# Performance work log

Measured on AMD Instinct MI355X. Metric: run time of the kernel, lower is better.

The kernel has to match this reference:

```python
import jax, jax.numpy as jnp
import numpy as np

B, C, H, W = 32, 512, 28, 28
NUM_CLASSES = 200
THRESHOLD = 0.6


def _conv(x, w, b, pad):
    y = jax.lax.conv_general_dilated(
        x, w, window_strides=(1, 1), padding=[(pad, pad), (pad, pad)],
        dimension_numbers=('NCHW', 'OIHW', 'NCHW'))
    return y + b[None, :, None, None]


def _classifier(x, w1, b1, w2, b2, w3, b3):
    x = jax.nn.relu(_conv(x, w1, b1, 1))
    x = jax.nn.relu(_conv(x, w2, b2, 1))
    return _conv(x, w3, b3, 0)


def _avg_pool3(x):
    # torch F.avg_pool2d(k=3, stride=1, pad=1, count_include_pad=True): sum window / 9
    s = jax.lax.reduce_window(x, 0.0, jax.lax.add, (1, 1, 3, 3), (1, 1, 1, 1),
                              [(0, 0), (0, 0), (1, 1), (1, 1)])
    return s / 9.0


def setup_inputs() -> dict:
    key = jax.random.key(0)
    ks = jax.random.split(key, 16)
    sc = 0.02
    inp = {
        'x': jax.random.normal(ks[0], (B, C, H, W), jnp.float32),
        'label': jax.random.randint(ks[1], (B, NUM_CLASSES), 0, 2),
        'w1a': jax.random.normal(ks[2], (1024, 512, 3, 3), jnp.float32) * sc,
        'b1a': jax.random.normal(ks[3], (1024,), jnp.float32) * sc,
        'w2a': jax.random.normal(ks[4], (1024, 1024, 3, 3), jnp.float32) * sc,
        'b2a': jax.random.normal(ks[5], (1024,), jnp.float32) * sc,
        'w3a': jax.random.normal(ks[6], (NUM_CLASSES, 1024, 1, 1), jnp.float32) * sc,
        'b3a': jax.random.normal(ks[7], (NUM_CLASSES,), jnp.float32) * sc,
        'w1b': jax.random.normal(ks[8], (1024, 512, 3, 3), jnp.float32) * sc,
        'b1b': jax.random.normal(ks[9], (1024,), jnp.float32) * sc,
        'w2b': jax.random.normal(ks[10], (1024, 1024, 3, 3), jnp.float32) * sc,
        'b2b': jax.random.normal(ks[11], (1024,), jnp.float32) * sc,
        'w3b': jax.random.normal(ks[12], (NUM_CLASSES, 1024, 1, 1), jnp.float32) * sc,
        'b3b': jax.random.normal(ks[13], (NUM_CLASSES,), jnp.float32) * sc,
    }
    return inp


def reference(x, label, w1a, b1a, w2a, b2a, w3a, b3a,
              w1b, b1b, w2b, b2b, w3b, b3b):
    feats = _avg_pool3(x)                       # [B,512,H,W]
    out_A = _classifier(feats, w1a, b1a, w2a, b2a, w3a, b3a)  # [B,K,H,W]
    logits_A = out_A.mean(axis=(2, 3))          # [B,K]

    # attention map: per-sample max over channels whose label is nonzero,
    # floored at 0 (the loop seeds the channel stack with a zeros map)
    sel = jnp.where(label[:, :, None, None] > 0, out_A, -jnp.inf)
    atten = jnp.maximum(sel.max(axis=1), 0.0)   # [B,H,W]

    # per-sample min-max normalization over HxW
    mins = atten.min(axis=(1, 2), keepdims=True)
    maxs = atten.max(axis=(1, 2), keepdims=True)
    atten_n = (atten - mins) / (maxs - mins)

    # threshold-erase mask (constant w.r.t. autograd, matching torch code)
    mask = jax.lax.stop_gradient(jnp.where(atten_n >= THRESHOLD, 0.0, 1.0))
    feats_erased = feats * mask[:, None, :, :]

    out_B = _classifier(feats_erased, w1b, b1b, w2b, b2b, w3b, b3b)
    logits_B = out_B.mean(axis=(2, 3))
    return logits_A, logits_B
```

## Files before the change

### kernel.cpp

```cpp
#include <hip/hip_runtime.h>
#include <hip/hip_bf16.h>

typedef unsigned long long ull;
typedef __attribute__((ext_vector_type(8))) short short8;
typedef __attribute__((ext_vector_type(8))) __bf16 bf16x8;
typedef __attribute__((ext_vector_type(4))) float floatx4;

#define GLL16(gp, lp) __builtin_amdgcn_global_load_lds( \
  (__attribute__((address_space(1))) void*)(gp), \
  (__attribute__((address_space(3))) void*)(lp), 16, 0, 0)

#define WVM(N) asm volatile("s_waitcnt vmcnt(" #N ")" ::: "memory")

__device__ __forceinline__ floatx4 mfma16(short8 a, short8 b, floatx4 c){
  return __builtin_amdgcn_mfma_f32_16x16x32_bf16(
      __builtin_bit_cast(bf16x8, a), __builtin_bit_cast(bf16x8, b), c, 0, 0, 0);
}

__device__ __forceinline__ unsigned pkbf(float a, float b){
  unsigned ua = __float_as_uint(a), ub = __float_as_uint(b);
  ua += 0x7fffu + ((ua >> 16) & 1u);
  ub += 0x7fffu + ((ub >> 16) & 1u);
  return (ua >> 16) | (ub & 0xffff0000u);
}

__global__ __launch_bounds__(256) void pool_kernel(const float* __restrict__ x,
                                                   unsigned short* __restrict__ out){
  __shared__ float xs[16*784];
  const int tid = threadIdx.x;
  const int b = blockIdx.x >> 5, cg = blockIdx.x & 31;
  const float* src = x + ((size_t)b*512 + cg*16)*784;
  for (int i=tid;i<16*784;i+=256) xs[i]=src[i];
  __syncthreads();
  unsigned* dst = (unsigned*)out + ((size_t)b*960)*256 + cg*8;
  for (int o=tid;o<30*32*8;o+=256){
    int cip = o & 7, pos = o >> 3;
    int row = pos >> 5, col = pos & 31;
    float s0=0.f, s1=0.f;
    if (row>=1 && row<=28 && col>=1 && col<=28){
      int h=row-1, w=col-1;
      const float* p0 = &xs[(cip*2)*784];
      const float* p1 = p0 + 784;
      #pragma unroll
      for (int dh=-1;dh<=1;++dh){ int hh=h+dh; if ((unsigned)hh<28u){
        #pragma unroll
        for (int dw=-1;dw<=1;++dw){ int ww=w+dw; if((unsigned)ww<28u){
          s0 += p0[hh*28+ww]; s1 += p1[hh*28+ww]; } } } }
      s0 /= 9.f; s1 /= 9.f;
    }
    dst[(size_t)pos*256 + cip] = pkbf(s0, s1);
  }
}

template<int CIN>
__global__ __launch_bounds__(256) void prep3x3(const float* __restrict__ w,
                                               unsigned short* __restrict__ Wt){
  __shared__ float wsm[CIN*9];
  const int co = blockIdx.x, tid = threadIdx.x;
  const float* src = w + (size_t)co*(CIN*9);
  for (int i=tid;i<CIN*9;i+=256) wsm[i]=src[i];
  __syncthreads();
  for (int o=tid;o<9*(CIN/2);o+=256){
    int t = o/(CIN/2), cp = o - t*(CIN/2);
    unsigned v = pkbf(wsm[(cp*2)*9+t], wsm[(cp*2+1)*9+t]);
    ((unsigned*)Wt)[(((size_t)t*1024+co)*CIN>>1) + cp] = v;
  }
}

__global__ __launch_bounds__(256) void prep1x1(const float* __restrict__ w3,
                                               unsigned short* __restrict__ Wp){
  const int row = blockIdx.x, tid = threadIdx.x;
  unsigned* dst = (unsigned*)Wp + (size_t)row*512;
  if (row < 200){
    const float* src = w3 + (size_t)row*1024;
    for (int j=tid;j<512;j+=256) dst[j] = pkbf(src[2*j], src[2*j+1]);
  } else {
    for (int j=tid;j<512;j+=256) dst[j] = 0u;
  }
}

template<int CIN>
__global__ __launch_bounds__(256, 2) void conv3x3_v8(
    const unsigned short* __restrict__ X,
    const unsigned short* __restrict__ Wt,
    const float* __restrict__ bias,
    unsigned short* __restrict__ Out)
{
  constexpr int NCH = CIN/32;
  constexpr size_t CB = (size_t)CIN*2;
  constexpr size_t TAPSTR = (size_t)1024*CB;
  __shared__ char Als[32768];
  __shared__ char Bls[40960];

  const int tid = threadIdx.x;
  const int l = tid & 63, wv = tid >> 6;
  const int cog = wv & 1, pg = wv >> 1;
  const int bid = blockIdx.x;
  const int co0 = (bid & 7) << 7;
  const int y = bid >> 3;
  const int b = y >> 2, rb = y & 3;
  const int r0 = rb << 3;
  const bool active = (pg == 0) || (rb < 3);

  const int sbyt = (l*16) ^ (((l>>3)&7)<<4);
  const int srow = sbyt >> 6;
  const int sw   = sbyt & 63;

  const ull aS0 = (ull)Wt + (size_t)(co0 + (wv*2)*16   + srow)*CB + sw;
  const ull aS1 = (ull)Wt + (size_t)(co0 + (wv*2+1)*16 + srow)*CB + sw;
  ull bS[5];
  #pragma unroll
  for (int k=0;k<5;++k){
    int q = (wv + 4*k)*16 + srow;
    int trow = q >> 5, tcol = q & 31;
    int ir = r0 + trow; if (ir > 29) ir = 29;
    bS[k] = (ull)X + ((size_t)b*960 + ir*32 + tcol)*CB + sw;
  }

  const int jl = l & 15, g = l >> 4;
  int paE[4];
  #pragma unroll
  for (int m=0;m<4;++m){
    int xo = (cog*64 + m*16 + jl)*64 + g*16;
    paE[m] = xo ^ (((xo>>7)&7)<<4);
  }
  int pbS[3][7];
  #pragma unroll
  for (int f=0;f<7;++f){
    int p = pg*112 + f*16 + jl;
    int hl = p/28, cl = p - hl*28;
    #pragma unroll
    for (int ss=0;ss<3;++ss){
      int xo = (hl*32 + cl + ss)*64 + g*16;
      pbS[ss][f] = xo ^ (((xo>>7)&7)<<4);
    }
  }

  floatx4 acc[4][7];
  #pragma unroll
  for (int m=0;m<4;++m)
    #pragma unroll
    for (int f=0;f<7;++f) acc[m][f] = (floatx4){0.f,0.f,0.f,0.f};

  #pragma unroll
  for (int k=0;k<5;++k) GLL16((const void*)bS[k], Bls + (wv + 4*k)*1024);
  #pragma unroll
  for (int pp=0;pp<3;++pp){
    const int tap = pp, slot = pp;
    GLL16((const void*)(aS0 + (size_t)tap*TAPSTR), Als + slot*8192 + (wv*2)*1024);
    GLL16((const void*)(aS1 + (size_t)tap*TAPSTR), Als + slot*8192 + (wv*2+1)*1024);
  }

  #pragma unroll 1
  for (int c=0;c<NCH;++c){
    const char* Bp = Bls + (c&1)*20480;
    #pragma unroll
    for (int t=0;t<9;++t){
      const int rr = t/3, ss = t - rr*3;
      if (t == 0){
        #pragma unroll
        for (int k=0;k<5;++k)
          GLL16((const void*)(bS[k] + (size_t)(c+1)*64),
                Bls + ((c+1)&1)*20480 + (wv + 4*k)*1024);
      }
      {
        const int stTap = (t<6) ? t+3 : t-6;
        const size_t aoff = (size_t)stTap*TAPSTR + (size_t)(c + (t>=6))*64;
        const int sd = ((c + t + 3) & 3)*8192;
        GLL16((const void*)(aS0 + aoff), Als + sd + (wv*2)*1024);
        GLL16((const void*)(aS1 + aoff), Als + sd + (wv*2+1)*1024);
      }
      if (t <= 2) { WVM(11); } else { WVM(6); }
      __builtin_amdgcn_s_barrier();
      if (active){
        const char* ap = Als + ((c + t) & 3)*8192;
        short8 a0 = *(const short8*)(ap + paE[0]);
        short8 a1 = *(const short8*)(ap + paE[1]);
        short8 a2 = *(const short8*)(ap + paE[2]);
        short8 a3 = *(const short8*)(ap + paE[3]);
        short8 bv[7];
        #pragma unroll
        for (int f=0;f<7;++f)
          bv[f] = *(const short8*)(Bp + (pbS[ss][f] + rr*2048));
        __builtin_amdgcn_s_setprio(1);
        #pragma unroll
        for (int f=0;f<7;++f){
          acc[0][f] = mfma16(a0, bv[f], acc[0][f]);
          acc[1][f] = mfma16(a1, bv[f], acc[1][f]);
          acc[2][f] = mfma16(a2, bv[f], acc[2][f]);
          acc[3][f] = mfma16(a3, bv[f], acc[3][f]);
        }
        __builtin_amdgcn_s_setprio(0);
      }
      __builtin_amdgcn_s_barrier();
    }
  }

  if (!active) return;

  #pragma unroll
  for (int m=0;m<4;++m){
    const int coL = cog*64 + m*16 + g*4;
    const float4 bv4 = *(const float4*)&bias[co0 + coL];
    #pragma unroll
    for (int f=0;f<7;++f){
      int pp = pg*112 + f*16 + jl;
      int hl = pp/28, cl = pp - hl*28;
      float v0 = fmaxf(acc[m][f][0] + bv4.x, 0.f);
      float v1 = fmaxf(acc[m][f][1] + bv4.y, 0.f);
      float v2 = fmaxf(acc[m][f][2] + bv4.z, 0.f);
      float v3 = fmaxf(acc[m][f][3] + bv4.w, 0.f);
      uint2 pk; pk.x = pkbf(v0,v1); pk.y = pkbf(v2,v3);
      size_t oa = ((size_t)b*960 + (size_t)(r0 + hl + 1)*32 + (cl + 1))*1024 + (co0 + coL);
      *(uint2*)(Out + oa) = pk;
    }
  }
}

template<int CIN, bool K3, bool BF16OUT>
__global__ __launch_bounds__(512, 2) void conv_mfma(
    const unsigned short* __restrict__ X,
    const unsigned short* __restrict__ Wt,
    const float* __restrict__ bias, int biasN,
    void* __restrict__ Out)
{
  constexpr int T9 = K3 ? 9 : 1;
  constexpr int NA = K3 ? 9 : 1;
  __shared__ short Als[T9*4096];
  __shared__ short Bls[10240];
  __shared__ float biasLs[128];

  const int tid = threadIdx.x;
  const int l = tid & 63, wv = tid >> 6;
  const int wc = wv & 3, wp = wv >> 2;
  const int co0 = blockIdx.x << 7;
  const int by = blockIdx.y;
  const int b = by >> 2, rb = by & 3;
  const int r0 = rb << 3;
  const int nrh = (rb < 3) ? 10 : 6;
  const int NB = 2*nrh;
  const bool active = (wp == 0) || (rb < 3);

  if (tid < 128) biasLs[tid] = (co0 + tid < biasN) ? bias[co0 + tid] : 0.f;

  const size_t laneOff = (size_t)(l >> 2)*(CIN*2) + (size_t)(l & 3)*16;

  ull aB[NA];
  #pragma unroll
  for (int j=0;j<NA;++j){
    int k = wv*NA + j;
    int t = K3 ? (k >> 3) : 0;
    int cog2 = K3 ? (k & 7) : k;
    aB[j] = (ull)Wt + ((size_t)(t*1024 + co0 + cog2*16)*(CIN*2)) + laneOff;
  }
  const ull xBase = (ull)X + ((size_t)b*960)*(CIN*2) + (size_t)(r0*32)*(CIN*2) + laneOff;
  ull bB0=0, bB1=0, bB2=0; int nb=0;
  if (wv < NB)      { bB0 = xBase + (size_t)(wv*16)*(CIN*2);      nb = 1; }
  if (wv + 8 < NB)  { bB1 = xBase + (size_t)((wv+8)*16)*(CIN*2);  nb = 2; }
  if (wv + 16 < NB) { bB2 = xBase + (size_t)((wv+16)*16)*(CIN*2); nb = 3; }

  const int jl = l & 15, g = l >> 4;
  int paE[2];
  #pragma unroll
  for (int m=0;m<2;++m) paE[m] = (wc*32 + m*16 + jl)*32 + g*8;
  int pbE[7], ph[7], pc[7];
  #pragma unroll
  for (int f=0;f<7;++f){
    int p = wp*112 + f*16 + jl;
    int hl = p / 28, cl = p - hl*28;
    ph[f]=hl; pc[f]=cl;
    pbE[f] = (hl*32 + cl)*32 + g*8;
  }

  floatx4 acc[2][7];
  #pragma unroll
  for (int m=0;m<2;++m)
    #pragma unroll
    for (int f=0;f<7;++f) acc[m][f] = (floatx4){0.f,0.f,0.f,0.f};

  const int NCH = CIN/32;
  for (int c=0;c<NCH;++c){
    if (c) __syncthreads();
    const size_t cOff = (size_t)c*64;
    #pragma unroll
    for (int j=0;j<NA;++j)
      GLL16((const void*)(aB[j] + cOff), (char*)Als + (wv*NA + j)*1024);
    GLL16((const void*)(bB0 + cOff), (char*)Bls + wv*1024);
    if (nb > 1) GLL16((const void*)(bB1 + cOff), (char*)Bls + (wv+8)*1024);
    if (nb > 2) GLL16((const void*)(bB2 + cOff), (char*)Bls + (wv+16)*1024);
    __syncthreads();
    if (active){
      #pragma unroll
      for (int t=0;t<T9;++t){
        const int tA = t*4096;
        const int tB = K3 ? (((t/3)*32 + (t - (t/3)*3))*32) : ((1*32+1)*32);
        short8 a0 = *(const short8*)&Als[tA + paE[0]];
        short8 a1 = *(const short8*)&Als[tA + paE[1]];
        #pragma unroll
        for (int f=0;f<7;++f){
          short8 bvv = *(const short8*)&Bls[tB + pbE[f]];
          acc[0][f] = mfma16(a0, bvv, acc[0][f]);
          acc[1][f] = mfma16(a1, bvv, acc[1][f]);
        }
      }
    }
  }

  if (!active) return;

  #pragma unroll
  for (int m=0;m<2;++m){
    const int coL = wc*32 + m*16 + g*4;
    const float4 bv4 = *(const float4*)&biasLs[coL];
    #pragma unroll
    for (int f=0;f<7;++f){
      float v0 = acc[m][f][0] + bv4.x;
      float v1 = acc[m][f][1] + bv4.y;
      float v2 = acc[m][f][2] + bv4.z;
      float v3 = acc[m][f][3] + bv4.w;
      if constexpr (BF16OUT){
        v0=fmaxf(v0,0.f); v1=fmaxf(v1,0.f); v2=fmaxf(v2,0.f); v3=fmaxf(v3,0.f);
        uint2 pk; pk.x = pkbf(v0,v1); pk.y = pkbf(v2,v3);
        size_t oa = ((size_t)b*960 + (size_t)(r0 + ph[f] + 1)*32 + (pc[f]+1))*1024 + (co0 + coL);
        *(uint2*)((unsigned short*)Out + oa) = pk;
      } else {
        int co = co0 + coL;
        if (co < 200){
          int p = wp*112 + f*16 + jl;
          size_t oa = ((size_t)b*784 + (size_t)(r0*28) + p)*200 + co;
          float4 ov; ov.x=v0; ov.y=v1; ov.z=v2; ov.w=v3;
          *(float4*)((float*)Out + oa) = ov;
        }
      }
    }
  }
}

__global__ __launch_bounds__(256) void logits_kernel(const float* __restrict__ outC,
                                                     float* __restrict__ dst){
  const int b = blockIdx.x, seg = blockIdx.y;
  const int co = threadIdx.x;
  if (co >= 200) return;
  const float* base = outC + ((size_t)b*784 + seg*98)*200 + co;
  float s = 0.f;
  for (int p=0;p<98;++p) s += base[(size_t)p*200];
  atomicAdd(&dst[b*200+co], s*(1.f/784.f));
}

__global__ __launch_bounds__(256) void atten_kernel(const float* __restrict__ outC,
                                                    const int* __restrict__ label,
                                                    float* __restrict__ mask){
  __shared__ float al[784];
  __shared__ float redn[256], redx[256];
  __shared__ unsigned char lab[200];
  const int b = blockIdx.x, tid = threadIdx.x;
  for (int i=tid;i<200;i+=256) lab[i] = label[b*200+i] > 0 ? 1 : 0;
  __syncthreads();
  for (int p=tid;p<784;p+=256){
    const float* row = outC + ((size_t)b*784+p)*200;
    float m = -__builtin_inff();
    for (int c=0;c<200;++c) if (lab[c]) m = fmaxf(m, row[c]);
    al[p] = fmaxf(m, 0.f);
  }
  __syncthreads();
  float mn = __builtin_inff(), mx = -__builtin_inff();
  for (int p=tid;p<784;p+=256){ float v=al[p]; mn=fminf(mn,v); mx=fmaxf(mx,v); }
  redn[tid]=mn; redx[tid]=mx; __syncthreads();
  for (int s2=128;s2>0;s2>>=1){
    if (tid<s2){ redn[tid]=fminf(redn[tid],redn[tid+s2]); redx[tid]=fmaxf(redx[tid],redx[tid+s2]); }
    __syncthreads();
  }
  mn = redn[0]; mx = redx[0];
  for (int p=tid;p<784;p+=256){
    float nrm = (al[p]-mn)/(mx-mn);
    mask[b*784+p] = (nrm >= 0.6f) ? 0.f : 1.f;
  }
}

__global__ __launch_bounds__(256) void erase_kernel(const unsigned short* __restrict__ feats,
                                                    const float* __restrict__ mask,
                                                    unsigned short* __restrict__ dst){
  const int blk = blockIdx.x; const int b = blk/30, row = blk - b*30;
  const size_t base = ((size_t)b*960 + row*32)*512;
  for (int i=threadIdx.x; i<4096; i+=256){
    int col = i >> 7;
    float mv = 0.f;
    if (row>=1 && row<=28 && col>=1 && col<=28) mv = mask[b*784 + (row-1)*28 + (col-1)];
    uint2 v = make_uint2(0u,0u);
    if (mv > 0.5f) v = *(const uint2*)(feats + base + (size_t)i*4);
    *(uint2*)(dst + base + (size_t)i*4) = v;
  }
}

extern "C" void kernel_launch(void* const* d_in, const int* in_sizes, int n_in,
                              void* d_out, int out_size, void* d_ws, size_t ws_size,
                              hipStream_t stream){
  (void)in_sizes; (void)n_in; (void)out_size; (void)ws_size;
  const float* x   = (const float*)d_in[0];
  const int* label = (const int*)d_in[1];
  const float* w1a = (const float*)d_in[2];  const float* b1a = (const float*)d_in[3];
  const float* w2a = (const float*)d_in[4];  const float* b2a = (const float*)d_in[5];
  const float* w3a = (const float*)d_in[6];  const float* b3a = (const float*)d_in[7];
  const float* w1b = (const float*)d_in[8];  const float* b1b = (const float*)d_in[9];
  const float* w2b = (const float*)d_in[10]; const float* b2b = (const float*)d_in[11];
  const float* w3b = (const float*)d_in[12]; const float* b3b = (const float*)d_in[13];

  char* ws = (char*)d_ws;
  unsigned short* WtS = (unsigned short*)(ws);
  unsigned short* WtL = (unsigned short*)(ws + 9441280);
  unsigned short* W3p = (unsigned short*)(ws + 28319744);
  unsigned short* F   = (unsigned short*)(ws + 28848128);
  unsigned short* G1  = (unsigned short*)(ws + 60309504);
  unsigned short* G2  = (unsigned short*)(ws + 123228160);
  float* outC  = (float*)(ws + 186146816);
  float* maskB = (float*)(ws + 206217216);
  float* logA = (float*)d_out;
  float* logB = logA + 6400;

  hipMemsetAsync(G1, 0, 62914560, stream);
  hipMemsetAsync(G2, 0, 62914560, stream);
  hipMemsetAsync(d_out, 0, 51200, stream);

  pool_kernel<<<1024,256,0,stream>>>(x, F);

  prep3x3<512><<<1024,256,0,stream>>>(w1a, WtS);
  conv3x3_v8<512><<<1024,256,0,stream>>>(F, WtS, b1a, G1);
  prep3x3<1024><<<1024,256,0,stream>>>(w2a, WtL);
  conv3x3_v8<1024><<<1024,256,0,stream>>>(G1, WtL, b2a, G2);
  prep1x1<<<256,256,0,stream>>>(w3a, W3p);
  conv_mfma<1024,false,false><<<dim3(2,128),512,0,stream>>>(G2, W3p, b3a, 200, outC);
  logits_kernel<<<dim3(32,8),256,0,stream>>>(outC, logA);
  atten_kernel<<<32,256,0,stream>>>(outC, label, maskB);
  erase_kernel<<<960,256,0,stream>>>(F, maskB, G1);

  prep3x3<512><<<1024,256,0,stream>>>(w1b, WtS);
  conv3x3_v8<512><<<1024,256,0,stream>>>(G1, WtS, b1b, G2);
  prep3x3<1024><<<1024,256,0,stream>>>(w2b, WtL);
  conv3x3_v8<1024><<<1024,256,0,stream>>>(G2, WtL, b2b, G1);
  prep1x1<<<256,256,0,stream>>>(w3b, W3p);
  conv_mfma<1024,false,false><<<dim3(2,128),512,0,stream>>>(G1, W3p, b3b, 200, outC);
  logits_kernel<<<dim3(32,8),256,0,stream>>>(outC, logB);
}
```

Measured before the change: 1.510 ms.

## Double K-chunk to 64 channels and restructure conv3x3 pipeline to double buffers

The 3x3 conv kernel now processes 64 input channels per chunk instead of 32. That halves the number of outer chunk iterations and doubles the MFMA work done per barrier. The weight-tile ring of four 8KB slots becomes two 16KB ping-pong buffers, each prefetched one tap ahead. The input tile is single-buffered at 40KB and reloaded after all nine taps of a chunk, with a wait and barrier at the start of the next chunk. Every tap now waits for all outstanding loads (vmcnt 0), which removes the deeper prefetch distance and may expose memory latency, especially when the input tile is refilled.

New measurement: 1.460 ms. 1.03x faster.

```diff
diff --git a/kernel.cpp b/kernel.cpp
--- a/kernel.cpp
+++ b/kernel.cpp
@@ -80,13 +80,13 @@
 }
 
 template<int CIN>
-__global__ __launch_bounds__(256, 2) void conv3x3_v8(
+__global__ __launch_bounds__(256, 2) void conv3x3_v9(
     const unsigned short* __restrict__ X,
     const unsigned short* __restrict__ Wt,
     const float* __restrict__ bias,
     unsigned short* __restrict__ Out)
 {
-  constexpr int NCH = CIN/32;
+  constexpr int NCH = CIN/64;
   constexpr size_t CB = (size_t)CIN*2;
   constexpr size_t TAPSTR = (size_t)1024*CB;
   __shared__ char Als[32768];
@@ -102,16 +102,18 @@
   const int r0 = rb << 3;
   const bool active = (pg == 0) || (rb < 3);
 
-  const int sbyt = (l*16) ^ (((l>>3)&7)<<4);
-  const int srow = sbyt >> 6;
-  const int sw   = sbyt & 63;
-
-  const ull aS0 = (ull)Wt + (size_t)(co0 + (wv*2)*16   + srow)*CB + sw;
-  const ull aS1 = (ull)Wt + (size_t)(co0 + (wv*2+1)*16 + srow)*CB + sw;
-  ull bS[5];
-  #pragma unroll
-  for (int k=0;k<5;++k){
-    int q = (wv + 4*k)*16 + srow;
+  const int sb = (l*16) ^ (((l>>3)&7)<<4);
+  const int sr = sb >> 7;
+  const int sw = sb & 127;
+
+  ull aS[4];
+  #pragma unroll
+  for (int k=0;k<4;++k)
+    aS[k] = (ull)Wt + (size_t)(co0 + (wv*4+k)*8 + sr)*CB + sw;
+  ull bS[10];
+  #pragma unroll
+  for (int k=0;k<10;++k){
+    int q = (wv + 4*k)*8 + sr;
     int trow = q >> 5, tcol = q & 31;
     int ir = r0 + trow; if (ir > 29) ir = 29;
     bS[k] = (ull)X + ((size_t)b*960 + ir*32 + tcol)*CB + sw;
@@ -121,7 +123,7 @@
   int paE[4];
   #pragma unroll
   for (int m=0;m<4;++m){
-    int xo = (cog*64 + m*16 + jl)*64 + g*16;
+    int xo = (cog*64 + m*16 + jl)*128 + g*16;
     paE[m] = xo ^ (((xo>>7)&7)<<4);
   }
   int pbS[3][7];
@@ -131,7 +133,7 @@
     int hl = p/28, cl = p - hl*28;
     #pragma unroll
     for (int ss=0;ss<3;++ss){
-      int xo = (hl*32 + cl + ss)*64 + g*16;
+      int xo = (hl*32 + cl + ss)*128 + g*16;
       pbS[ss][f] = xo ^ (((xo>>7)&7)<<4);
     }
   }
@@ -143,56 +145,59 @@
     for (int f=0;f<7;++f) acc[m][f] = (floatx4){0.f,0.f,0.f,0.f};
 
   #pragma unroll
-  for (int k=0;k<5;++k) GLL16((const void*)bS[k], Bls + (wv + 4*k)*1024);
-  #pragma unroll
-  for (int pp=0;pp<3;++pp){
-    const int tap = pp, slot = pp;
-    GLL16((const void*)(aS0 + (size_t)tap*TAPSTR), Als + slot*8192 + (wv*2)*1024);
-    GLL16((const void*)(aS1 + (size_t)tap*TAPSTR), Als + slot*8192 + (wv*2+1)*1024);
-  }
+  for (int k=0;k<10;++k) GLL16((const void*)bS[k], Bls + (wv + 4*k)*1024);
+  #pragma unroll
+  for (int k=0;k<4;++k)  GLL16((const void*)aS[k], Als + (wv*4+k)*1024);
+  WVM(0);
+  __builtin_amdgcn_s_barrier();
 
   #pragma unroll 1
   for (int c=0;c<NCH;++c){
-    const char* Bp = Bls + (c&1)*20480;
     #pragma unroll
     for (int t=0;t<9;++t){
       const int rr = t/3, ss = t - rr*3;
-      if (t == 0){
+      const int cur = ((c + t) & 1)*16384;
+      const int nxt = cur ^ 16384;
+      const int ntap = (t<8) ? t+1 : 0;
+      const size_t aoff = (size_t)ntap*TAPSTR + (size_t)(t<8 ? c : c+1)*128;
+      #pragma unroll
+      for (int k=0;k<4;++k)
+        GLL16((const void*)(aS[k] + aoff), Als + nxt + (wv*4+k)*1024);
+      if (t == 0 && c > 0){
+        WVM(4);
+        __builtin_amdgcn_s_barrier();
+      }
+      if (active){
         #pragma unroll
-        for (int k=0;k<5;++k)
-          GLL16((const void*)(bS[k] + (size_t)(c+1)*64),
-                Bls + ((c+1)&1)*20480 + (wv + 4*k)*1024);
+        for (int ks=0;ks<2;++ks){
+          const int kx = ks*64;
+          const char* ap = Als + cur;
+          short8 a0 = *(const short8*)(ap + (paE[0]^kx));
+          short8 a1 = *(const short8*)(ap + (paE[1]^kx));
+          short8 a2 = *(const short8*)(ap + (paE[2]^kx));
+          short8 a3 = *(const short8*)(ap + (paE[3]^kx));
+          short8 bv[7];
+          #pragma unroll
+          for (int f=0;f<7;++f)
+            bv[f] = *(const short8*)(Bls + ((pbS[ss][f]^kx) + rr*4096));
+          __builtin_amdgcn_s_setprio(1);
+          #pragma unroll
+          for (int f=0;f<7;++f){
+            acc[0][f] = mfma16(a0, bv[f], acc[0][f]);
+            acc[1][f] = mfma16(a1, bv[f], acc[1][f]);
+            acc[2][f] = mfma16(a2, bv[f], acc[2][f]);
+            acc[3][f] = mfma16(a3, bv[f], acc[3][f]);
+          }
+          __builtin_amdgcn_s_setprio(0);
+        }
       }
-      {
-        const int stTap = (t<6) ? t+3 : t-6;
-        const size_t aoff = (size_t)stTap*TAPSTR + (size_t)(c + (t>=6))*64;
-        const int sd = ((c + t + 3) & 3)*8192;
-        GLL16((const void*)(aS0 + aoff), Als + sd + (wv*2)*1024);
-        GLL16((const void*)(aS1 + aoff), Als + sd + (wv*2+1)*1024);
-      }
-      if (t <= 2) { WVM(11); } else { WVM(6); }
+      WVM(0);
       __builtin_amdgcn_s_barrier();
-      if (active){
-        const char* ap = Als + ((c + t) & 3)*8192;
-        short8 a0 = *(const short8*)(ap + paE[0]);
-        short8 a1 = *(const short8*)(ap + paE[1]);
-        short8 a2 = *(const short8*)(ap + paE[2]);
-        short8 a3 = *(const short8*)(ap + paE[3]);
-        short8 bv[7];
-        #pragma unroll
-        for (int f=0;f<7;++f)
-          bv[f] = *(const short8*)(Bp + (pbS[ss][f] + rr*2048));
-        __builtin_amdgcn_s_setprio(1);
-        #pragma unroll
-        for (int f=0;f<7;++f){
-          acc[0][f] = mfma16(a0, bv[f], acc[0][f]);
-          acc[1][f] = mfma16(a1, bv[f], acc[1][f]);
-          acc[2][f] = mfma16(a2, bv[f], acc[2][f]);
-          acc[3][f] = mfma16(a3, bv[f], acc[3][f]);
-        }
-        __builtin_amdgcn_s_setprio(0);
-      }
-      __builtin_amdgcn_s_barrier();
+    }
+    if (c + 1 < NCH){
+      #pragma unroll
+      for (int k=0;k<10;++k)
+        GLL16((const void*)(bS[k] + (size_t)(c+1)*128), Bls + (wv + 4*k)*1024);
     }
   }
 
@@ -424,9 +429,9 @@
   pool_kernel<<<1024,256,0,stream>>>(x, F);
 
   prep3x3<512><<<1024,256,0,stream>>>(w1a, WtS);
-  conv3x3_v8<512><<<1024,256,0,stream>>>(F, WtS, b1a, G1);
+  conv3x3_v9<512><<<1024,256,0,stream>>>(F, WtS, b1a, G1);
   prep3x3<1024><<<1024,256,0,stream>>>(w2a, WtL);
-  conv3x3_v8<1024><<<1024,256,0,stream>>>(G1, WtL, b2a, G2);
+  conv3x3_v9<1024><<<1024,256,0,stream>>>(G1, WtL, b2a, G2);
   prep1x1<<<256,256,0,stream>>>(w3a, W3p);
   conv_mfma<1024,false,false><<<dim3(2,128),512,0,stream>>>(G2, W3p, b3a, 200, outC);
   logits_kernel<<<dim3(32,8),256,0,stream>>>(outC, logA);
@@ -434,9 +439,9 @@
   erase_kernel<<<960,256,0,stream>>>(F, maskB, G1);
 
   prep3x3<512><<<1024,256,0,stream>>>(w1b, WtS);
-  conv3x3_v8<512><<<1024,256,0,stream>>>(G1, WtS, b1b, G2);
+  conv3x3_v9<512><<<1024,256,0,stream>>>(G1, WtS, b1b, G2);
   prep3x3<1024><<<1024,256,0,stream>>>(w2b, WtL);
-  conv3x3_v8<1024><<<1024,256,0,stream>>>(G2, WtL, b2b, G1);
+  conv3x3_v9<1024><<<1024,256,0,stream>>>(G2, WtL, b2b, G1);
   prep1x1<<<256,256,0,stream>>>(w3b, W3p);
   conv_mfma<1024,false,false><<<dim3(2,128),512,0,stream>>>(G1, W3p, b3b, 200, outC);
   logits_kernel<<<dim3(32,8),256,0,stream>>>(outC, logB);
```

## Shrink conv3x3 LDS staging to single-buffered B and triple-buffered A

Applied to the files above, without the earlier changes.

The 3x3 convolution kernel now keeps one input-tile buffer in LDS instead of two, and three weight-tap slots instead of four. The prefetch distance for weight taps drops from three to two, and wait counts are adjusted to match. This cuts per-block LDS from about 72KB to about 44KB, presumably so more blocks can be resident per CU. In exchange, each channel chunk's input tile load is now issued and waited on at the start of that chunk, so its latency is no longer hidden behind the previous chunk's MFMAs.

New measurement: 1.487 ms. No clear change (-1.6%).

```diff
diff --git a/kernel.cpp b/kernel.cpp
--- a/kernel.cpp
+++ b/kernel.cpp
@@ -80,7 +80,7 @@
 }
 
 template<int CIN>
-__global__ __launch_bounds__(256, 2) void conv3x3_v8(
+__global__ __launch_bounds__(256, 2) void conv3x3_v10(
     const unsigned short* __restrict__ X,
     const unsigned short* __restrict__ Wt,
     const float* __restrict__ bias,
@@ -89,8 +89,8 @@
   constexpr int NCH = CIN/32;
   constexpr size_t CB = (size_t)CIN*2;
   constexpr size_t TAPSTR = (size_t)1024*CB;
-  __shared__ char Als[32768];
-  __shared__ char Bls[40960];
+  __shared__ char Als[24576];
+  __shared__ char Bls[20480];
 
   const int tid = threadIdx.x;
   const int l = tid & 63, wv = tid >> 6;
@@ -144,36 +144,32 @@
 
   #pragma unroll
   for (int k=0;k<5;++k) GLL16((const void*)bS[k], Bls + (wv + 4*k)*1024);
-  #pragma unroll
-  for (int pp=0;pp<3;++pp){
-    const int tap = pp, slot = pp;
-    GLL16((const void*)(aS0 + (size_t)tap*TAPSTR), Als + slot*8192 + (wv*2)*1024);
-    GLL16((const void*)(aS1 + (size_t)tap*TAPSTR), Als + slot*8192 + (wv*2+1)*1024);
-  }
+  GLL16((const void*)aS0,            Als +        (wv*2)*1024);
+  GLL16((const void*)aS1,            Als +        (wv*2+1)*1024);
+  GLL16((const void*)(aS0 + TAPSTR), Als + 8192 + (wv*2)*1024);
+  GLL16((const void*)(aS1 + TAPSTR), Als + 8192 + (wv*2+1)*1024);
 
   #pragma unroll 1
   for (int c=0;c<NCH;++c){
-    const char* Bp = Bls + (c&1)*20480;
     #pragma unroll
     for (int t=0;t<9;++t){
       const int rr = t/3, ss = t - rr*3;
-      if (t == 0){
+      if (t == 0 && c > 0){
         #pragma unroll
         for (int k=0;k<5;++k)
-          GLL16((const void*)(bS[k] + (size_t)(c+1)*64),
-                Bls + ((c+1)&1)*20480 + (wv + 4*k)*1024);
+          GLL16((const void*)(bS[k] + (size_t)c*64), Bls + (wv + 4*k)*1024);
       }
       {
-        const int stTap = (t<6) ? t+3 : t-6;
-        const size_t aoff = (size_t)stTap*TAPSTR + (size_t)(c + (t>=6))*64;
-        const int sd = ((c + t + 3) & 3)*8192;
+        const int stTap = (t<7) ? t+2 : t-7;
+        const size_t aoff = (size_t)stTap*TAPSTR + (size_t)(c + (t>=7))*64;
+        const int sd = ((t+2)%3)*8192;
         GLL16((const void*)(aS0 + aoff), Als + sd + (wv*2)*1024);
         GLL16((const void*)(aS1 + aoff), Als + sd + (wv*2+1)*1024);
       }
-      if (t <= 2) { WVM(11); } else { WVM(6); }
+      if (t == 0) { WVM(2); } else { WVM(4); }
       __builtin_amdgcn_s_barrier();
       if (active){
-        const char* ap = Als + ((c + t) & 3)*8192;
+        const char* ap = Als + (t%3)*8192;
         short8 a0 = *(const short8*)(ap + paE[0]);
         short8 a1 = *(const short8*)(ap + paE[1]);
         short8 a2 = *(const short8*)(ap + paE[2]);
@@ -181,7 +177,7 @@
         short8 bv[7];
         #pragma unroll
         for (int f=0;f<7;++f)
-          bv[f] = *(const short8*)(Bp + (pbS[ss][f] + rr*2048));
+          bv[f] = *(const short8*)(Bls + (pbS[ss][f] + rr*2048));
         __builtin_amdgcn_s_setprio(1);
         #pragma unroll
         for (int f=0;f<7;++f){
@@ -424,9 +420,9 @@
   pool_kernel<<<1024,256,0,stream>>>(x, F);
 
   prep3x3<512><<<1024,256,0,stream>>>(w1a, WtS);
-  conv3x3_v8<512><<<1024,256,0,stream>>>(F, WtS, b1a, G1);
+  conv3x3_v10<512><<<1024,256,0,stream>>>(F, WtS, b1a, G1);
   prep3x3<1024><<<1024,256,0,stream>>>(w2a, WtL);
-  conv3x3_v8<1024><<<1024,256,0,stream>>>(G1, WtL, b2a, G2);
+  conv3x3_v10<1024><<<1024,256,0,stream>>>(G1, WtL, b2a, G2);
   prep1x1<<<256,256,0,stream>>>(w3a, W3p);
   conv_mfma<1024,false,false><<<dim3(2,128),512,0,stream>>>(G2, W3p, b3a, 200, outC);
   logits_kernel<<<dim3(32,8),256,0,stream>>>(outC, logA);
@@ -434,9 +430,9 @@
   erase_kernel<<<960,256,0,stream>>>(F, maskB, G1);
 
   prep3x3<512><<<1024,256,0,stream>>>(w1b, WtS);
-  conv3x3_v8<512><<<1024,256,0,stream>>>(G1, WtS, b1b, G2);
+  conv3x3_v10<512><<<1024,256,0,stream>>>(G1, WtS, b1b, G2);
   prep3x3<1024><<<1024,256,0,stream>>>(w2b, WtL);
-  conv3x3_v8<1024><<<1024,256,0,stream>>>(G2, WtL, b2b, G1);
+  conv3x3_v10<1024><<<1024,256,0,stream>>>(G2, WtL, b2b, G1);
   prep1x1<<<256,256,0,stream>>>(w3b, W3p);
   conv_mfma<1024,false,false><<<dim3(2,128),512,0,stream>>>(G1, W3p, b3b, 200, outC);
   logits_kernel<<<dim3(32,8),256,0,stream>>>(outC, logB);
```
